# Performance work log

Hardware: AMD Instinct MI355X
Metric: run time of the kernel (lower is better)

Reference implementation:

```python
import jax, jax.numpy as jnp
import numpy as np

N_WORD = 50000
N_DOC = 10000
E_WW = 800000
E_WD = 320000


def _sage(h_src, h_dst, src, dst, n_dst, W_self, W_neigh, b):
    # DGL SAGEConv('mean'): fc_self(h_dst) + fc_neigh(mean_{u in N(v)} h_u) + bias
    ones = jnp.ones((src.shape[0],), dtype=h_src.dtype)
    deg = jax.ops.segment_sum(ones, dst, num_segments=n_dst)            # [n_dst]
    agg = jax.ops.segment_sum(h_src[src], dst, num_segments=n_dst)      # [n_dst, d]
    mean = agg / jnp.maximum(deg, 1.0)[:, None]                          # zero for isolated
    return h_dst @ W_self + mean @ W_neigh + b


def _layer(xw, xd, edges, Ws, Wn, b):
    (ww_s, ww_d, wwr_s, wwr_d, wd_s, wd_d, wdr_s, wdr_d) = edges
    # relations targeting 'word': word2word, word2wordr, word2documentr
    h_ww = _sage(xw, xw, ww_s, ww_d, N_WORD, Ws[0], Wn[0], b[0])
    h_wwr = _sage(xw, xw, wwr_s, wwr_d, N_WORD, Ws[1], Wn[1], b[1])
    h_wdr = _sage(xd, xw, wdr_s, wdr_d, N_WORD, Ws[3], Wn[3], b[3])
    # relation targeting 'document': word2document
    h_wd = _sage(xw, xd, wd_s, wd_d, N_DOC, Ws[2], Wn[2], b[2])
    # HeteroGraphConv aggregate='stack' then torch.sum(dim=1) == sum over relations; then relu
    return jax.nn.relu(h_ww + h_wwr + h_wdr), jax.nn.relu(h_wd)


def setup_inputs() -> dict:
    key = jax.random.key(0)
    ks = jax.random.split(key, 20)
    d_in, d_h = 256, 128
    inp = {
        "x_word": jax.random.normal(ks[0], (N_WORD, d_in), jnp.float32),
        "x_doc": jax.random.normal(ks[1], (N_DOC, d_in), jnp.float32),
        "ww_src": jax.random.randint(ks[2], (E_WW,), 0, N_WORD, jnp.int32),
        "ww_dst": jax.random.randint(ks[3], (E_WW,), 0, N_WORD, jnp.int32),
        "wwr_src": jax.random.randint(ks[4], (E_WW,), 0, N_WORD, jnp.int32),
        "wwr_dst": jax.random.randint(ks[5], (E_WW,), 0, N_WORD, jnp.int32),
        "wd_src": jax.random.randint(ks[6], (E_WD,), 0, N_WORD, jnp.int32),
        "wd_dst": jax.random.randint(ks[7], (E_WD,), 0, N_DOC, jnp.int32),
        "wdr_src": jax.random.randint(ks[8], (E_WD,), 0, N_DOC, jnp.int32),
        "wdr_dst": jax.random.randint(ks[9], (E_WD,), 0, N_WORD, jnp.int32),
        "Wself1": jax.random.normal(ks[10], (4, d_in, d_h), jnp.float32) * (1.0 / np.sqrt(d_in)),
        "Wneigh1": jax.random.normal(ks[11], (4, d_in, d_h), jnp.float32) * (1.0 / np.sqrt(d_in)),
        "b1": jnp.zeros((4, d_h), jnp.float32),
        "Wself2": jax.random.normal(ks[12], (4, d_h, d_h), jnp.float32) * (1.0 / np.sqrt(d_h)),
        "Wneigh2": jax.random.normal(ks[13], (4, d_h, d_h), jnp.float32) * (1.0 / np.sqrt(d_h)),
        "b2": jnp.zeros((4, d_h), jnp.float32),
        "lin_w": jax.random.normal(ks[14], (1, d_h), jnp.float32) * (1.0 / np.sqrt(d_h)),
        "lin_b": jnp.ones((1,), jnp.float32),
    }
    return inp


def reference(x_word, x_doc, ww_src, ww_dst, wwr_src, wwr_dst, wd_src, wd_dst,
              wdr_src, wdr_dst, Wself1, Wneigh1, b1, Wself2, Wneigh2, b2, lin_w, lin_b):
    edges = (ww_src, ww_dst, wwr_src, wwr_dst, wd_src, wd_dst, wdr_src, wdr_dst)
    xw, xd = _layer(x_word, x_doc, edges, Wself1, Wneigh1, b1)
    xw, xd = _layer(xw, xd, edges, Wself2, Wneigh2, b2)
    out_w = jax.nn.sigmoid(xw @ lin_w.T + lin_b)  # [N_WORD, 1]
    out_d = jax.nn.sigmoid(xd @ lin_w.T + lin_b)  # [N_DOC, 1]
    return out_w, out_d
```

## Files before the change

kernel.cpp:

```cpp
#include <hip/hip_runtime.h>
#include <math.h>

#define N_WORD 50000
#define N_DOC  10000
#define E_WW   800000
#define E_WD   320000
#define D_IN   256
#define D_H    128

#define NPB    256
#define NBK_W  196
#define NBK_D  40
#define BKT    (3 * NBK_W + NBK_D)
#define EPB    8192
#define NBLK_WW 98
#define NBLK_WD 40
#define NBLK_TOT (2 * NBLK_WW + 2 * NBLK_WD)
#define PACK_BLKS 145

#define CAP_WW  4736
#define CAP_WDR 2176
#define CAP_WD  8960

#define WSTRIP ((N_WORD + 63) / 64)
#define DSTRIP ((N_DOC + 63) / 64)
#define NSTRIP (WSTRIP + DSTRIP)

typedef __attribute__((ext_vector_type(8))) short short8;
typedef __attribute__((ext_vector_type(4))) float f32x4;
typedef __attribute__((ext_vector_type(2))) float f32x2;

__device__ inline unsigned short f2bf(float f) {
  unsigned u = __float_as_uint(f);
  u = (u + 0x7fffu + ((u >> 16) & 1u)) >> 16;
  return (unsigned short)u;
}

__device__ inline float bflo(unsigned u) { return __uint_as_float(u << 16); }
__device__ inline float bfhi(unsigned u) { return __uint_as_float(u & 0xffff0000u); }

struct G6 { const short* B[6]; unsigned short* C[6]; };

template <int ABF, int K>
__device__ void gemm_body(const void* __restrict__ Aw, const void* __restrict__ Ad,
                          const G6& g, int blk) {
  constexpr int KT = K >> 5;
  int wid = threadIdx.x >> 6, lane = threadIdx.x & 63;
  const void* A; int M, row0, h0, h1;
  if (blk < WSTRIP) { A = Aw; M = N_WORD; row0 = blk << 6; h0 = 0; h1 = 4; }
  else { A = Ad; M = N_DOC; row0 = (blk - WSTRIP) << 6; h0 = 4; h1 = 6; }
  int r = lane & 15, quad = lane >> 4;
  int m0 = row0 + wid * 16;
  int mA = m0 + r; if (mA >= M) mA = M - 1;
  short8 afr[KT];
  if (ABF) {
    const short* ap = (const short*)A + (size_t)mA * K + quad * 8;
#pragma unroll
    for (int kt = 0; kt < KT; ++kt) afr[kt] = *(const short8*)(ap + kt * 32);
  } else {
    const float* ap = (const float*)A + (size_t)mA * K + quad * 8;
#pragma unroll
    for (int kt = 0; kt < KT; ++kt) {
      float4 a0 = *(const float4*)(ap + kt * 32);
      float4 a1 = *(const float4*)(ap + kt * 32 + 4);
      short8 v;
      v[0] = (short)f2bf(a0.x); v[1] = (short)f2bf(a0.y);
      v[2] = (short)f2bf(a0.z); v[3] = (short)f2bf(a0.w);
      v[4] = (short)f2bf(a1.x); v[5] = (short)f2bf(a1.y);
      v[6] = (short)f2bf(a1.z); v[7] = (short)f2bf(a1.w);
      afr[kt] = v;
    }
  }
#pragma unroll
  for (int kt = 0; kt < KT; ++kt) asm volatile("" : "+v"(afr[kt]));
  for (int h = h0; h < h1; ++h) {
    const short* Bp = g.B[h];
    f32x4 acc[8];
#pragma unroll
    for (int nt = 0; nt < 8; ++nt) acc[nt] = (f32x4){0.f, 0.f, 0.f, 0.f};
#pragma unroll
    for (int kt = 0; kt < KT; ++kt) {
      const short* bbase = Bp + ((size_t)kt * 4096) + lane * 8;
#pragma unroll
      for (int nt = 0; nt < 8; ++nt) {
        short8 bf = *(const short8*)(bbase + (size_t)nt * 512);
        acc[nt] = __builtin_amdgcn_mfma_f32_16x16x32_bf16(afr[kt], bf, acc[nt], 0, 0, 0);
      }
    }
    unsigned short* C = g.C[h];
#pragma unroll
    for (int nt = 0; nt < 8; ++nt)
#pragma unroll
      for (int rr = 0; rr < 4; ++rr) {
        int row = m0 + quad * 4 + rr;
        if (row < M) C[(size_t)row * 128 + nt * 16 + r] = f2bf(acc[nt][rr]);
      }
  }
}

__global__ __launch_bounds__(256, 2) void gemm1_kernel(
    const void* __restrict__ Aw, const void* __restrict__ Ad, G6 g) {
  gemm_body<0, 256>(Aw, Ad, g, blockIdx.x);
}

__global__ __launch_bounds__(256, 2) void gemm2_kernel(
    const void* __restrict__ Aw, const void* __restrict__ Ad, G6 g) {
  gemm_body<1, 128>(Aw, Ad, g, blockIdx.x);
}

__device__ inline void rel_map(int b, const int* wwd, const int* wwrd, const int* wdrd,
                               const int* wdd, const int*& dst, int& E, int& gbase, int& lb) {
  if (b < NBLK_WW) { dst = wwd; E = E_WW; gbase = 0; lb = b; }
  else if (b < 2 * NBLK_WW) { dst = wwrd; E = E_WW; gbase = NBK_W; lb = b - NBLK_WW; }
  else if (b < 2 * NBLK_WW + NBLK_WD) { dst = wdrd; E = E_WD; gbase = 2 * NBK_W; lb = b - 2 * NBLK_WW; }
  else { dst = wdd; E = E_WD; gbase = 3 * NBK_W; lb = b - 2 * NBLK_WW - NBLK_WD; }
}

struct BinLDS {
  unsigned buf[EPB];
  int hist[NBK_W];
  int lofs[NBK_W];
  int gofs[NBK_W];
  int lcur[NBK_W];
  int sm[256];
};

__device__ void bin_body(int b, BinLDS& L,
    const int* wws, const int* wwd, const int* wwrs, const int* wwrd,
    const int* wdrs, const int* wdrd, const int* wds, const int* wdd,
    int* bcnt, unsigned* st_ww, unsigned* st_wwr, unsigned* st_wdr, unsigned* st_wd) {
  const int* dst; int E, gbase, lb;
  rel_map(b, wwd, wwrd, wdrd, wdd, dst, E, gbase, lb);
  const int* src; unsigned* st; int cap;
  if (b < NBLK_WW) { src = wws; st = st_ww; cap = CAP_WW; }
  else if (b < 2 * NBLK_WW) { src = wwrs; st = st_wwr; cap = CAP_WW; }
  else if (b < 2 * NBLK_WW + NBLK_WD) { src = wdrs; st = st_wdr; cap = CAP_WDR; }
  else { src = wds; st = st_wd; cap = CAP_WD; }
  int tid = threadIdx.x;
  int e0 = lb * EPB;
  int ecnt = E - e0; if (ecnt > EPB) ecnt = EPB;
  if (tid < NBK_W) L.hist[tid] = 0;
  __syncthreads();
  int dcache[EPB / 256];
#pragma unroll
  for (int k = 0; k < EPB / 256; ++k) {
    int i = e0 + k * 256 + tid;
    int d = (i < E) ? dst[i] : -1;
    dcache[k] = d;
    if (d >= 0) atomicAdd(&L.hist[d >> 8], 1);
  }
  __syncthreads();
  {
    int v = (tid < NBK_W) ? L.hist[tid] : 0;
    L.sm[tid] = v;
    __syncthreads();
    for (int o = 1; o < 256; o <<= 1) {
      int add = (tid >= o) ? L.sm[tid - o] : 0;
      __syncthreads();
      L.sm[tid] += add;
      __syncthreads();
    }
    if (tid < NBK_W) {
      int ex = L.sm[tid] - v;
      L.lofs[tid] = ex;
      L.lcur[tid] = ex;
      int base = v ? atomicAdd(&bcnt[gbase + tid], v) : 0;
      L.gofs[tid] = (int)((size_t)tid * cap) + base - ex;
    }
  }
  __syncthreads();
#pragma unroll
  for (int k = 0; k < EPB / 256; ++k) {
    int d = dcache[k];
    if (d >= 0) {
      int i = e0 + k * 256 + tid;
      int bk = d >> 8;
      int p = atomicAdd(&L.lcur[bk], 1);
      L.buf[p] = ((unsigned)bk << 24) | ((unsigned)(d & 255) << 16) |
                 (unsigned)(src[i] & 0xFFFF);
    }
  }
  __syncthreads();
#pragma unroll
  for (int k = 0; k < EPB / 256; ++k) {
    int p = k * 256 + tid;
    if (p < ecnt) {
      unsigned e = L.buf[p];
      st[L.gofs[e >> 24] + p] = e & 0x00FFFFFFu;
    }
  }
}

__global__ __launch_bounds__(256, 4) void prepbin_kernel(
    const float* __restrict__ Ws1, const float* __restrict__ Wn1,
    const float* __restrict__ Ws2, const float* __restrict__ Wn2,
    short* __restrict__ Bp1, short* __restrict__ Bp2,
    const float* __restrict__ b1, const float* __restrict__ b2,
    float* __restrict__ bs1, float* __restrict__ bs2,
    unsigned* __restrict__ zA, unsigned* __restrict__ zB,
    unsigned* __restrict__ zC, unsigned* __restrict__ zD,
    const int* wws, const int* wwd, const int* wwrs, const int* wwrd,
    const int* wdrs, const int* wdrd, const int* wds, const int* wdd,
    int* bcnt, unsigned* st_ww, unsigned* st_wwr, unsigned* st_wdr, unsigned* st_wd) {
  __shared__ BinLDS L;
  int b = blockIdx.x;
  if (b > PACK_BLKS) {
    bin_body(b - PACK_BLKS - 1, L, wws, wwd, wwrs, wwrd, wdrs, wdrd, wds, wdd,
             bcnt, st_ww, st_wwr, st_wdr, st_wd);
    return;
  }
  if (b == PACK_BLKS) {
    if (threadIdx.x < 64) {
      zA[(size_t)N_WORD * 64 + threadIdx.x] = 0;
      zB[(size_t)N_WORD * 64 + threadIdx.x] = 0;
      zC[(size_t)N_WORD * 64 + threadIdx.x] = 0;
      zD[(size_t)N_DOC * 64 + threadIdx.x] = 0;
    }
    return;
  }
  int tid = b * 256 + threadIdx.x;
  const int L1T = 6 * 4096;
  const int L2T = 6 * 2048;
  if (tid >= L1T + L2T) {
    int t = tid - (L1T + L2T);
    if (t < 128) bs1[t] = b1[t] + b1[128 + t] + b1[384 + t];
    else if (t < 256) { int u = t - 128; bs2[u] = b2[u] + b2[128 + u] + b2[384 + u]; }
    return;
  }
  const float *src0, *src1 = nullptr, *src2 = nullptr;
  short* dstp;
  int kt, nt, lane;
  if (tid < L1T) {
    int mat = tid / 4096, rem = tid % 4096;
    kt = rem / 512; nt = (rem / 64) % 8; lane = rem % 64;
    const int W1 = 256 * 128;
    if (mat == 0) { src0 = Ws1; src1 = Ws1 + W1; src2 = Ws1 + 3 * W1; }
    else if (mat <= 4) src0 = Wn1 + (size_t)(mat - 1) * W1;
    else src0 = Ws1 + 2 * W1;
    dstp = Bp1 + (size_t)mat * W1 + ((size_t)(kt * 8 + nt) * 64 + lane) * 8;
  } else {
    int t2 = tid - L1T;
    int mat = t2 / 2048, rem = t2 % 2048;
    kt = rem / 512; nt = (rem / 64) % 8; lane = rem % 64;
    const int W2 = 128 * 128;
    if (mat == 0) { src0 = Ws2; src1 = Ws2 + W2; src2 = Ws2 + 3 * W2; }
    else if (mat <= 4) src0 = Wn2 + (size_t)(mat - 1) * W2;
    else src0 = Ws2 + 2 * W2;
    dstp = Bp2 + (size_t)mat * W2 + ((size_t)(kt * 8 + nt) * 64 + lane) * 8;
  }
  int n = nt * 16 + (lane & 15);
  int kb = kt * 32 + (lane >> 4) * 8;
  short8 v;
#pragma unroll
  for (int j = 0; j < 8; ++j) {
    float f = src0[(size_t)(kb + j) * 128 + n];
    if (src1) f += src1[(size_t)(kb + j) * 128 + n] + src2[(size_t)(kb + j) * 128 + n];
    v[j] = (short)f2bf(f);
  }
  *(short8*)dstp = v;
}

struct CSRB {
  const unsigned *st_ww, *st_wwr, *st_wdr, *st_wd;
  unsigned short *c_ww, *c_wwr, *c_wdr, *c_wd;
  int *rp_ww, *rp_wwr, *rp_wdr, *rp_wd;
  const int* bcnt;
};

__global__ __launch_bounds__(256) void place_kernel(CSRB q) {
  __shared__ int cnt[256], off[256], sm[256];
  int g = blockIdx.x;
  const unsigned* st; unsigned short* csr; int* rp; int relFirst, relLast, n, cap, Etot;
  if (g < NBK_W)            { st = q.st_ww;  csr = q.c_ww;  rp = q.rp_ww;  relFirst = 0;         relLast = NBK_W - 1;     n = N_WORD; cap = CAP_WW;  Etot = E_WW; }
  else if (g < 2 * NBK_W)   { st = q.st_wwr; csr = q.c_wwr; rp = q.rp_wwr; relFirst = NBK_W;     relLast = 2 * NBK_W - 1; n = N_WORD; cap = CAP_WW;  Etot = E_WW; }
  else if (g < 3 * NBK_W)   { st = q.st_wdr; csr = q.c_wdr; rp = q.rp_wdr; relFirst = 2 * NBK_W; relLast = 3 * NBK_W - 1; n = N_WORD; cap = CAP_WDR; Etot = E_WD; }
  else                      { st = q.st_wd;  csr = q.c_wd;  rp = q.rp_wd;  relFirst = 3 * NBK_W; relLast = BKT - 1;       n = N_DOC;  cap = CAP_WD;  Etot = E_WD; }
  int cb = g - relFirst;
  int tid = threadIdx.x;
  int v = (tid < cb) ? q.bcnt[relFirst + tid] : 0;
  sm[tid] = v;
  __syncthreads();
  for (int o = 128; o > 0; o >>= 1) {
    if (tid < o) sm[tid] += sm[tid + o];
    __syncthreads();
  }
  int bstart = sm[0];
  if (g == relLast && tid == 0) rp[n] = Etot;
  __syncthreads();
  int node_base = cb << 8;
  int node_cnt = n - node_base; if (node_cnt > NPB) node_cnt = NPB;
  int ecnt = q.bcnt[g];
  const unsigned* w = st + (size_t)cb * cap;
  cnt[tid] = 0;
  __syncthreads();
  for (int j = tid; j < ecnt; j += 256) atomicAdd(&cnt[w[j] >> 16], 1);
  __syncthreads();
  int c = cnt[tid];
  sm[tid] = c;
  __syncthreads();
  for (int o = 1; o < 256; o <<= 1) {
    int add = (tid >= o) ? sm[tid - o] : 0;
    __syncthreads();
    sm[tid] += add;
    __syncthreads();
  }
  int ex = sm[tid] - c;
  off[tid] = ex;
  if (tid < node_cnt) rp[node_base + tid] = bstart + ex;
  __syncthreads();
  for (int j = tid; j < ecnt; j += 256) {
    unsigned e = w[j];
    int p = atomicAdd(&off[e >> 16], 1);
    csr[bstart + p] = (unsigned short)(e & 0xFFFFu);
  }
}

__device__ inline void accum_rel4(const uint4* __restrict__ Y,
                                  const unsigned short* __restrict__ csr,
                                  int beg, int end, int lane, int r, int g,
                                  int zrow, f32x2* __restrict__ f) {
  int deg = end - beg;
  if (deg <= 0) return;
  f32x2 a0 = {0.f, 0.f}, a1 = a0, a2 = a0, a3 = a0;
  for (int base = beg; base < end; base += 64) {
    int cnt = end - base; if (cnt > 64) cnt = 64;
    int ld = base + lane;
    int idx = (ld < end) ? (int)csr[ld] : zrow;
    for (int j = 0; j < cnt; j += 16) {
      uint4 u[4];
#pragma unroll
      for (int t = 0; t < 4; ++t) {
        int sv = __shfl(idx, j + (t << 2) + g, 64);
        u[t] = Y[(unsigned)((sv << 4) + r)];
      }
#pragma unroll
      for (int t = 0; t < 4; ++t) {
        a0 += (f32x2){bflo(u[t].x), bfhi(u[t].x)};
        a1 += (f32x2){bflo(u[t].y), bfhi(u[t].y)};
        a2 += (f32x2){bflo(u[t].z), bfhi(u[t].z)};
        a3 += (f32x2){bflo(u[t].w), bfhi(u[t].w)};
      }
    }
  }
  float inv = 1.0f / (float)deg;
  f[0] += a0 * inv; f[1] += a1 * inv; f[2] += a2 * inv; f[3] += a3 * inv;
}

__global__ __launch_bounds__(256) void gather_all(
    const unsigned* __restrict__ y_ww, const unsigned* __restrict__ y_wwr,
    const unsigned* __restrict__ y_wdr, const unsigned* __restrict__ y_wd,
    const unsigned short* __restrict__ c_ww, const unsigned short* __restrict__ c_wwr,
    const unsigned short* __restrict__ c_wdr, const unsigned short* __restrict__ c_wd,
    const int* __restrict__ r_ww, const int* __restrict__ r_wwr,
    const int* __restrict__ r_wdr, const int* __restrict__ r_wd,
    const unsigned* __restrict__ tW, const unsigned* __restrict__ tD,
    const float* __restrict__ bW, const float* __restrict__ bD,
    const float* __restrict__ lw, const float* __restrict__ lb,
    unsigned* __restrict__ oW16, unsigned* __restrict__ oD16,
    float* __restrict__ oF, int mode) {
  int gn = (blockIdx.x << 2) + (threadIdx.x >> 6);
  if (gn >= N_WORD + N_DOC) return;
  int lane = threadIdx.x & 63;
  int r = lane & 15, g = lane >> 4;
  f32x2 f[4];
#pragma unroll
  for (int i = 0; i < 4; ++i) f[i] = (f32x2){0.f, 0.f};
  bool isw = (gn < N_WORD);
  int node = isw ? gn : gn - N_WORD;
  if (isw) {
    accum_rel4((const uint4*)y_ww, c_ww, r_ww[node], r_ww[node + 1], lane, r, g, N_WORD, f);
    accum_rel4((const uint4*)y_wwr, c_wwr, r_wwr[node], r_wwr[node + 1], lane, r, g, N_WORD, f);
    accum_rel4((const uint4*)y_wdr, c_wdr, r_wdr[node], r_wdr[node + 1], lane, r, g, N_DOC, f);
  } else {
    accum_rel4((const uint4*)y_wd, c_wd, r_wd[node], r_wd[node + 1], lane, r, g, N_WORD, f);
  }
#pragma unroll
  for (int i = 0; i < 4; ++i) {
    f[i].x += __shfl_xor(f[i].x, 16, 64);
    f[i].y += __shfl_xor(f[i].y, 16, 64);
    f[i].x += __shfl_xor(f[i].x, 32, 64);
    f[i].y += __shfl_xor(f[i].y, 32, 64);
  }
  const unsigned* tS = isw ? tW : tD;
  uint4 tu = ((const uint4*)tS)[(unsigned)((node << 4) + r)];
  const float* bs = isw ? bW : bD;
  float4 bv0 = ((const float4*)bs)[2 * r];
  float4 bv1 = ((const float4*)bs)[2 * r + 1];
  f[0].x = fmaxf(f[0].x + bflo(tu.x) + bv0.x, 0.f);
  f[0].y = fmaxf(f[0].y + bfhi(tu.x) + bv0.y, 0.f);
  f[1].x = fmaxf(f[1].x + bflo(tu.y) + bv0.z, 0.f);
  f[1].y = fmaxf(f[1].y + bfhi(tu.y) + bv0.w, 0.f);
  f[2].x = fmaxf(f[2].x + bflo(tu.z) + bv1.x, 0.f);
  f[2].y = fmaxf(f[2].y + bfhi(tu.z) + bv1.y, 0.f);
  f[3].x = fmaxf(f[3].x + bflo(tu.w) + bv1.z, 0.f);
  f[3].y = fmaxf(f[3].y + bfhi(tu.w) + bv1.w, 0.f);
  if (mode == 1) {
    if (g == 0) {
      uint4 pk;
      pk.x = (unsigned)f2bf(f[0].x) | ((unsigned)f2bf(f[0].y) << 16);
      pk.y = (unsigned)f2bf(f[1].x) | ((unsigned)f2bf(f[1].y) << 16);
      pk.z = (unsigned)f2bf(f[2].x) | ((unsigned)f2bf(f[2].y) << 16);
      pk.w = (unsigned)f2bf(f[3].x) | ((unsigned)f2bf(f[3].y) << 16);
      unsigned* o = isw ? oW16 : oD16;
      ((uint4*)o)[(unsigned)((node << 4) + r)] = pk;
    }
  } else {
    float4 lv0 = ((const float4*)lw)[2 * r];
    float4 lv1 = ((const float4*)lw)[2 * r + 1];
    float s = f[0].x * lv0.x + f[0].y * lv0.y + f[1].x * lv0.z + f[1].y * lv0.w +
              f[2].x * lv1.x + f[2].y * lv1.y + f[3].x * lv1.z + f[3].y * lv1.w;
#pragma unroll
    for (int off = 8; off > 0; off >>= 1) s += __shfl_xor(s, off, 64);
    if (lane == 0) oF[isw ? node : N_WORD + node] = 1.0f / (1.0f + expf(-(s + lb[0])));
  }
}

extern "C" void kernel_launch(void* const* d_in, const int* in_sizes, int n_in,
                              void* d_out, int out_size, void* d_ws, size_t ws_size,
                              hipStream_t stream) {
  const float* xw      = (const float*)d_in[0];
  const float* xd      = (const float*)d_in[1];
  const int*   ww_src  = (const int*)d_in[2];
  const int*   ww_dst  = (const int*)d_in[3];
  const int*   wwr_src = (const int*)d_in[4];
  const int*   wwr_dst = (const int*)d_in[5];
  const int*   wd_src  = (const int*)d_in[6];
  const int*   wd_dst  = (const int*)d_in[7];
  const int*   wdr_src = (const int*)d_in[8];
  const int*   wdr_dst = (const int*)d_in[9];
  const float* Ws1     = (const float*)d_in[10];
  const float* Wn1     = (const float*)d_in[11];
  const float* b1      = (const float*)d_in[12];
  const float* Ws2     = (const float*)d_in[13];
  const float* Wn2     = (const float*)d_in[14];
  const float* b2      = (const float*)d_in[15];
  const float* lin_w   = (const float*)d_in[16];
  const float* lin_b   = (const float*)d_in[17];
  float* out = (float*)d_out;

  char* p = (char*)d_ws;
  auto alloc = [&](size_t nbytes) {
    char* r = p;
    p += (nbytes + 255) & ~(size_t)255;
    return r;
  };
  unsigned* twA  = (unsigned*)alloc((size_t)N_WORD * D_H * 2);
  unsigned* tdA  = (unsigned*)alloc((size_t)N_DOC * D_H * 2);
  unsigned* xw1B = (unsigned*)alloc((size_t)N_WORD * D_H * 2 + 256);
  unsigned* xd1B = (unsigned*)alloc((size_t)N_DOC * D_H * 2);
  unsigned* yB0 = (unsigned*)alloc((size_t)N_WORD * D_H * 2);
  unsigned* yB1 = (unsigned*)alloc(((size_t)NBK_W * CAP_WDR + (size_t)NBK_D * CAP_WD) * 4);
  unsigned* yB2 = (unsigned*)alloc((size_t)N_WORD * D_H * 2 + 256);
  unsigned* ydB = (unsigned*)alloc((size_t)N_DOC * D_H * 2 + 256);
  unsigned short* csr_ww  = (unsigned short*)alloc((size_t)E_WW * 2);
  unsigned short* csr_wwr = (unsigned short*)alloc((size_t)E_WW * 2);
  unsigned short* csr_wdr = (unsigned short*)alloc((size_t)E_WD * 2);
  unsigned short* csr_wd  = (unsigned short*)alloc((size_t)E_WD * 2);
  int* rp_ww  = (int*)alloc((size_t)(N_WORD + 1) * 4);
  int* rp_wwr = (int*)alloc((size_t)(N_WORD + 1) * 4);
  int* rp_wdr = (int*)alloc((size_t)(N_WORD + 1) * 4);
  int* rp_wd  = (int*)alloc((size_t)(N_DOC + 1) * 4);
  short* Bp1 = (short*)alloc((size_t)6 * 256 * 128 * 2);
  short* Bp2 = (short*)alloc((size_t)6 * 128 * 128 * 2);
  int* bcnt  = (int*)alloc((size_t)BKT * 4);
  float* bs1 = (float*)alloc(D_H * 4);
  float* bs2 = (float*)alloc(D_H * 4);
  unsigned* yBX = (unsigned*)alloc((size_t)N_WORD * D_H * 2 + 256);
  unsigned* st_ww  = yB0;
  unsigned* st_wwr = st_ww + (size_t)NBK_W * CAP_WW;
  unsigned* st_wdr = yB1;
  unsigned* st_wd  = st_wdr + (size_t)NBK_W * CAP_WDR;

  const int W1 = 256 * 128;
  const int W2 = 128 * 128;

  hipMemsetAsync(bcnt, 0, (size_t)BKT * 4, stream);

  prepbin_kernel<<<PACK_BLKS + 1 + NBLK_TOT, 256, 0, stream>>>(
      Ws1, Wn1, Ws2, Wn2, Bp1, Bp2, b1, b2, bs1, bs2,
      yB2, xw1B, yBX, ydB,
      ww_src, ww_dst, wwr_src, wwr_dst, wdr_src, wdr_dst, wd_src, wd_dst,
      bcnt, st_ww, st_wwr, st_wdr, st_wd);

  G6 g1;
  g1.B[0] = Bp1 + 0 * W1; g1.C[0] = (unsigned short*)twA;
  g1.B[1] = Bp1 + 1 * W1; g1.C[1] = (unsigned short*)yB2;
  g1.B[2] = Bp1 + 2 * W1; g1.C[2] = (unsigned short*)xw1B;
  g1.B[3] = Bp1 + 3 * W1; g1.C[3] = (unsigned short*)yBX;
  g1.B[4] = Bp1 + 5 * W1; g1.C[4] = (unsigned short*)tdA;
  g1.B[5] = Bp1 + 4 * W1; g1.C[5] = (unsigned short*)ydB;
  gemm1_kernel<<<NSTRIP, 256, 0, stream>>>(xw, xd, g1);

  CSRB q;
  q.st_ww = st_ww; q.st_wwr = st_wwr; q.st_wdr = st_wdr; q.st_wd = st_wd;
  q.c_ww = csr_ww; q.c_wwr = csr_wwr; q.c_wdr = csr_wdr; q.c_wd = csr_wd;
  q.rp_ww = rp_ww; q.rp_wwr = rp_wwr; q.rp_wdr = rp_wdr; q.rp_wd = rp_wd;
  q.bcnt = bcnt;
  place_kernel<<<BKT, 256, 0, stream>>>(q);

  gather_all<<<(N_WORD + N_DOC + 3) / 4, 256, 0, stream>>>(
      yB2, xw1B, ydB, yBX, csr_ww, csr_wwr, csr_wdr, csr_wd,
      rp_ww, rp_wwr, rp_wdr, rp_wd, twA, tdA, bs1, b1 + 256,
      lin_w, lin_b, yB0, xd1B, nullptr, 1);

  G6 g2;
  g2.B[0] = Bp2 + 0 * W2; g2.C[0] = (unsigned short*)twA;
  g2.B[1] = Bp2 + 1 * W2; g2.C[1] = (unsigned short*)yB2;
  g2.B[2] = Bp2 + 2 * W2; g2.C[2] = (unsigned short*)xw1B;
  g2.B[3] = Bp2 + 3 * W2; g2.C[3] = (unsigned short*)yBX;
  g2.B[4] = Bp2 + 5 * W2; g2.C[4] = (unsigned short*)tdA;
  g2.B[5] = Bp2 + 4 * W2; g2.C[5] = (unsigned short*)ydB;
  gemm2_kernel<<<NSTRIP, 256, 0, stream>>>(yB0, xd1B, g2);

  gather_all<<<(N_WORD + N_DOC + 3) / 4, 256, 0, stream>>>(
      yB2, xw1B, ydB, yBX, csr_ww, csr_wwr, csr_wdr, csr_wd,
      rp_ww, rp_wwr, rp_wdr, rp_wd, twA, tdA, bs2, b2 + 256,
      lin_w, lin_b, nullptr, nullptr, out, 2);
}
```

Measured before the change: 406.3 us.

## Fuse edge binning into first GEMM launch and fold counter zeroing into prep

Edge binning moves out of the weight-packing kernel and into the first GEMM launch, so binning blocks and GEMM strips run side by side in one grid. The bucket-counter memset is replaced by zeroing inside the prep kernel, which removes one stream operation. The intent is to overlap the memory-bound binning with the MFMA GEMM and cut launch count. In exchange, the fused kernel carries the large binning LDS struct and a 4-blocks-per-CU launch bound, which may reduce occupancy or register budget for the GEMM blocks.

```diff
diff --git a/kernel.cpp b/kernel.cpp
--- a/kernel.cpp
+++ b/kernel.cpp
@@ -98,118 +98,22 @@
   }
 }
 
-__global__ __launch_bounds__(256, 2) void gemm1_kernel(
-    const void* __restrict__ Aw, const void* __restrict__ Ad, G6 g) {
-  gemm_body<0, 256>(Aw, Ad, g, blockIdx.x);
-}
-
 __global__ __launch_bounds__(256, 2) void gemm2_kernel(
     const void* __restrict__ Aw, const void* __restrict__ Ad, G6 g) {
   gemm_body<1, 128>(Aw, Ad, g, blockIdx.x);
 }
 
-__device__ inline void rel_map(int b, const int* wwd, const int* wwrd, const int* wdrd,
-                               const int* wdd, const int*& dst, int& E, int& gbase, int& lb) {
-  if (b < NBLK_WW) { dst = wwd; E = E_WW; gbase = 0; lb = b; }
-  else if (b < 2 * NBLK_WW) { dst = wwrd; E = E_WW; gbase = NBK_W; lb = b - NBLK_WW; }
-  else if (b < 2 * NBLK_WW + NBLK_WD) { dst = wdrd; E = E_WD; gbase = 2 * NBK_W; lb = b - 2 * NBLK_WW; }
-  else { dst = wdd; E = E_WD; gbase = 3 * NBK_W; lb = b - 2 * NBLK_WW - NBLK_WD; }
-}
-
-struct BinLDS {
-  unsigned buf[EPB];
-  int hist[NBK_W];
-  int lofs[NBK_W];
-  int gofs[NBK_W];
-  int lcur[NBK_W];
-  int sm[256];
-};
-
-__device__ void bin_body(int b, BinLDS& L,
-    const int* wws, const int* wwd, const int* wwrs, const int* wwrd,
-    const int* wdrs, const int* wdrd, const int* wds, const int* wdd,
-    int* bcnt, unsigned* st_ww, unsigned* st_wwr, unsigned* st_wdr, unsigned* st_wd) {
-  const int* dst; int E, gbase, lb;
-  rel_map(b, wwd, wwrd, wdrd, wdd, dst, E, gbase, lb);
-  const int* src; unsigned* st; int cap;
-  if (b < NBLK_WW) { src = wws; st = st_ww; cap = CAP_WW; }
-  else if (b < 2 * NBLK_WW) { src = wwrs; st = st_wwr; cap = CAP_WW; }
-  else if (b < 2 * NBLK_WW + NBLK_WD) { src = wdrs; st = st_wdr; cap = CAP_WDR; }
-  else { src = wds; st = st_wd; cap = CAP_WD; }
-  int tid = threadIdx.x;
-  int e0 = lb * EPB;
-  int ecnt = E - e0; if (ecnt > EPB) ecnt = EPB;
-  if (tid < NBK_W) L.hist[tid] = 0;
-  __syncthreads();
-  int dcache[EPB / 256];
-#pragma unroll
-  for (int k = 0; k < EPB / 256; ++k) {
-    int i = e0 + k * 256 + tid;
-    int d = (i < E) ? dst[i] : -1;
-    dcache[k] = d;
-    if (d >= 0) atomicAdd(&L.hist[d >> 8], 1);
-  }
-  __syncthreads();
-  {
-    int v = (tid < NBK_W) ? L.hist[tid] : 0;
-    L.sm[tid] = v;
-    __syncthreads();
-    for (int o = 1; o < 256; o <<= 1) {
-      int add = (tid >= o) ? L.sm[tid - o] : 0;
-      __syncthreads();
-      L.sm[tid] += add;
-      __syncthreads();
-    }
-    if (tid < NBK_W) {
-      int ex = L.sm[tid] - v;
-      L.lofs[tid] = ex;
-      L.lcur[tid] = ex;
-      int base = v ? atomicAdd(&bcnt[gbase + tid], v) : 0;
-      L.gofs[tid] = (int)((size_t)tid * cap) + base - ex;
-    }
-  }
-  __syncthreads();
-#pragma unroll
-  for (int k = 0; k < EPB / 256; ++k) {
-    int d = dcache[k];
-    if (d >= 0) {
-      int i = e0 + k * 256 + tid;
-      int bk = d >> 8;
-      int p = atomicAdd(&L.lcur[bk], 1);
-      L.buf[p] = ((unsigned)bk << 24) | ((unsigned)(d & 255) << 16) |
-                 (unsigned)(src[i] & 0xFFFF);
-    }
-  }
-  __syncthreads();
-#pragma unroll
-  for (int k = 0; k < EPB / 256; ++k) {
-    int p = k * 256 + tid;
-    if (p < ecnt) {
-      unsigned e = L.buf[p];
-      st[L.gofs[e >> 24] + p] = e & 0x00FFFFFFu;
-    }
-  }
-}
-
-__global__ __launch_bounds__(256, 4) void prepbin_kernel(
+__global__ __launch_bounds__(256) void prep_kernel(
     const float* __restrict__ Ws1, const float* __restrict__ Wn1,
     const float* __restrict__ Ws2, const float* __restrict__ Wn2,
     short* __restrict__ Bp1, short* __restrict__ Bp2,
     const float* __restrict__ b1, const float* __restrict__ b2,
-    float* __restrict__ bs1, float* __restrict__ bs2,
+    float* __restrict__ bs1, float* __restrict__ bs2, int* __restrict__ bcnt,
     unsigned* __restrict__ zA, unsigned* __restrict__ zB,
-    unsigned* __restrict__ zC, unsigned* __restrict__ zD,
-    const int* wws, const int* wwd, const int* wwrs, const int* wwrd,
-    const int* wdrs, const int* wdrd, const int* wds, const int* wdd,
-    int* bcnt, unsigned* st_ww, unsigned* st_wwr, unsigned* st_wdr, unsigned* st_wd) {
-  __shared__ BinLDS L;
+    unsigned* __restrict__ zC, unsigned* __restrict__ zD) {
   int b = blockIdx.x;
-  if (b > PACK_BLKS) {
-    bin_body(b - PACK_BLKS - 1, L, wws, wwd, wwrs, wwrd, wdrs, wdrd, wds, wdd,
-             bcnt, st_ww, st_wwr, st_wdr, st_wd);
-    return;
-  }
   if (b == PACK_BLKS) {
+    for (int i = threadIdx.x; i < BKT; i += 256) bcnt[i] = 0;
     if (threadIdx.x < 64) {
       zA[(size_t)N_WORD * 64 + threadIdx.x] = 0;
       zB[(size_t)N_WORD * 64 + threadIdx.x] = 0;
@@ -258,6 +162,96 @@
     v[j] = (short)f2bf(f);
   }
   *(short8*)dstp = v;
+}
+
+__device__ inline void rel_map(int b, const int* wwd, const int* wwrd, const int* wdrd,
+                               const int* wdd, const int*& dst, int& E, int& gbase, int& lb) {
+  if (b < NBLK_WW) { dst = wwd; E = E_WW; gbase = 0; lb = b; }
+  else if (b < 2 * NBLK_WW) { dst = wwrd; E = E_WW; gbase = NBK_W; lb = b - NBLK_WW; }
+  else if (b < 2 * NBLK_WW + NBLK_WD) { dst = wdrd; E = E_WD; gbase = 2 * NBK_W; lb = b - 2 * NBLK_WW; }
+  else { dst = wdd; E = E_WD; gbase = 3 * NBK_W; lb = b - 2 * NBLK_WW - NBLK_WD; }
+}
+
+struct BinLDS {
+  unsigned buf[EPB];
+  int hist[NBK_W];
+  int lofs[NBK_W];
+  int gofs[NBK_W];
+  int lcur[NBK_W];
+  int sm[256];
+};
+
+__global__ __launch_bounds__(256, 4) void bin_gemm1(
+    const int* wws, const int* wwd, const int* wwrs, const int* wwrd,
+    const int* wdrs, const int* wdrd, const int* wds, const int* wdd,
+    int* bcnt, unsigned* st_ww, unsigned* st_wwr, unsigned* st_wdr, unsigned* st_wd,
+    const float* __restrict__ Aw, const float* __restrict__ Ad, G6 g) {
+  __shared__ BinLDS L;
+  int b = blockIdx.x;
+  if (b >= NBLK_TOT) {
+    gemm_body<0, 256>(Aw, Ad, g, b - NBLK_TOT);
+    return;
+  }
+  const int* dst; int E, gbase, lb;
+  rel_map(b, wwd, wwrd, wdrd, wdd, dst, E, gbase, lb);
+  const int* src; unsigned* st; int cap;
+  if (b < NBLK_WW) { src = wws; st = st_ww; cap = CAP_WW; }
+  else if (b < 2 * NBLK_WW) { src = wwrs; st = st_wwr; cap = CAP_WW; }
+  else if (b < 2 * NBLK_WW + NBLK_WD) { src = wdrs; st = st_wdr; cap = CAP_WDR; }
+  else { src = wds; st = st_wd; cap = CAP_WD; }
+  int tid = threadIdx.x;
+  int e0 = lb * EPB;
+  int ecnt = E - e0; if (ecnt > EPB) ecnt = EPB;
+  if (tid < NBK_W) L.hist[tid] = 0;
+  __syncthreads();
+  int dcache[EPB / 256];
+#pragma unroll
+  for (int k = 0; k < EPB / 256; ++k) {
+    int i = e0 + k * 256 + tid;
+    int d = (i < E) ? dst[i] : -1;
+    dcache[k] = d;
+    if (d >= 0) atomicAdd(&L.hist[d >> 8], 1);
+  }
+  __syncthreads();
+  {
+    int v = (tid < NBK_W) ? L.hist[tid] : 0;
+    L.sm[tid] = v;
+    __syncthreads();
+    for (int o = 1; o < 256; o <<= 1) {
+      int add = (tid >= o) ? L.sm[tid - o] : 0;
+      __syncthreads();
+      L.sm[tid] += add;
+      __syncthreads();
+    }
+    if (tid < NBK_W) {
+      int ex = L.sm[tid] - v;
+      L.lofs[tid] = ex;
+      L.lcur[tid] = ex;
+      int base = v ? atomicAdd(&bcnt[gbase + tid], v) : 0;
+      L.gofs[tid] = (int)((size_t)tid * cap) + base - ex;
+    }
+  }
+  __syncthreads();
+#pragma unroll
+  for (int k = 0; k < EPB / 256; ++k) {
+    int d = dcache[k];
+    if (d >= 0) {
+      int i = e0 + k * 256 + tid;
+      int bk = d >> 8;
+      int p = atomicAdd(&L.lcur[bk], 1);
+      L.buf[p] = ((unsigned)bk << 24) | ((unsigned)(d & 255) << 16) |
+                 (unsigned)(src[i] & 0xFFFF);
+    }
+  }
+  __syncthreads();
+#pragma unroll
+  for (int k = 0; k < EPB / 256; ++k) {
+    int p = k * 256 + tid;
+    if (p < ecnt) {
+      unsigned e = L.buf[p];
+      st[L.gofs[e >> 24] + p] = e & 0x00FFFFFFu;
+    }
+  }
 }
 
 struct CSRB {
@@ -474,13 +468,9 @@
   const int W1 = 256 * 128;
   const int W2 = 128 * 128;
 
-  hipMemsetAsync(bcnt, 0, (size_t)BKT * 4, stream);
-
-  prepbin_kernel<<<PACK_BLKS + 1 + NBLK_TOT, 256, 0, stream>>>(
-      Ws1, Wn1, Ws2, Wn2, Bp1, Bp2, b1, b2, bs1, bs2,
-      yB2, xw1B, yBX, ydB,
-      ww_src, ww_dst, wwr_src, wwr_dst, wdr_src, wdr_dst, wd_src, wd_dst,
-      bcnt, st_ww, st_wwr, st_wdr, st_wd);
+  prep_kernel<<<PACK_BLKS + 1, 256, 0, stream>>>(
+      Ws1, Wn1, Ws2, Wn2, Bp1, Bp2, b1, b2, bs1, bs2, bcnt,
+      yB2, xw1B, yBX, ydB);
 
   G6 g1;
   g1.B[0] = Bp1 + 0 * W1; g1.C[0] = (unsigned short*)twA;
@@ -489,7 +479,9 @@
   g1.B[3] = Bp1 + 3 * W1; g1.C[3] = (unsigned short*)yBX;
   g1.B[4] = Bp1 + 5 * W1; g1.C[4] = (unsigned short*)tdA;
   g1.B[5] = Bp1 + 4 * W1; g1.C[5] = (unsigned short*)ydB;
-  gemm1_kernel<<<NSTRIP, 256, 0, stream>>>(xw, xd, g1);
+  bin_gemm1<<<NBLK_TOT + NSTRIP, 256, 0, stream>>>(
+      ww_src, ww_dst, wwr_src, wwr_dst, wdr_src, wdr_dst, wd_src, wd_dst,
+      bcnt, st_ww, st_wwr, st_wdr, st_wd, xw, xd, g1);
 
   CSRB q;
   q.st_ww = st_ww; q.st_wwr = st_wwr; q.st_wdr = st_wdr; q.st_wd = st_wd;
```

Result: faster. 383.4 us (-5.6%).
